# Kernel tuning notes

Measured on AMD Instinct MI355X. Metric: run time of the kernel, lower is better.

## Reference

```python
import jax, jax.numpy as jnp
import numpy as np

B, N, K_H, K_EC = 32, 2048, 50, 5  # graphs, nodes/graph, homophily-knn k, edgeconv k


def _leaky(v):
    return jnp.where(v >= 0, v, 0.01 * v)


def _pairwise_sq(xg):
    # xg: [B,N,F] -> squared euclidean distances [B,N,N]
    s = jnp.sum(xg * xg, axis=-1)
    return s[:, :, None] + s[:, None, :] - 2.0 * jnp.einsum('bnf,bmf->bnm', xg, xg)


def _gather(xg, idx):
    # xg [B,N,F], idx [B,N,k] -> [B,N,k,F]
    return jax.vmap(lambda xs, ix: xs[ix])(xg, idx)


def _edge_conv(xg, w1, b1, w2, b2):
    # DynamicEdgeConv: knn (self included, as PyG knn), msg = nn([x_i, x_j - x_i]), aggr='add'
    d = _pairwise_sq(xg)
    _, idx = jax.lax.top_k(-d, K_EC)          # [B,N,k]
    xj = _gather(xg, idx)                      # [B,N,k,F]
    xi = jnp.broadcast_to(xg[:, :, None, :], xj.shape)
    m = jnp.concatenate([xi, xj - xi], axis=-1)
    h = _leaky(m @ w1 + b1)
    h = _leaky(h @ w2 + b2)
    return h.sum(axis=2)                       # add aggregation -> [B,N,out]


def _homophily(y, idx):
    # y [B,N], idx [B,N,k]: fraction of edges whose endpoints have equal value, per graph
    yj = jax.vmap(lambda ys, ix: ys[ix])(y, idx)
    same = (yj == y[:, :, None]).astype(jnp.float32)
    return same.mean(axis=(1, 2))              # [B]


def reference(x, pos, batch, c1w1, c1b1, c1w2, c1b2, c2w1, c2b1, c2w2, c2b2,
              l1w1, l1b1, l1w2, l1b2, mw1, mb1, mw2, mb2):
    xx = jnp.concatenate([x, pos], axis=1).reshape(B, N, 4)
    # homophily kNN graph (k=50, self-loops excluded as in knn_graph)
    d = _pairwise_sq(xx) + jnp.eye(N, dtype=xx.dtype) * 1e9
    _, hidx = jax.lax.top_k(-d, K_H)
    h = [_homophily(xx[..., c], hidx) for c in range(4)]  # hx,hy,hz,hq each [B]
    x1 = _edge_conv(xx, c1w1, c1b1, c1w2, c1b2)   # [B,N,64]
    x2 = _edge_conv(x1, c2w1, c2b1, c2w2, c2b2)   # shared conv2 weights
    x3 = _edge_conv(x2, c2w1, c2b1, c2w2, c2b2)
    feat = jnp.concatenate([xx, x1, x2, x3], axis=-1)  # [B,N,196]
    o = _leaky(feat @ l1w1 + l1b1) @ l1w2 + l1b2       # lin1 -> [B,N,256]
    o = o.mean(axis=1)                                  # global_mean_pool -> [B,256]
    o = jnp.concatenate([o] + [hh[:, None] for hh in h], axis=1)  # [B,260]
    o = _leaky(o)
    o = _leaky(o @ mw1 + mb1)
    return o @ mw2 + mb2                                # [B,cla]


def setup_inputs() -> dict:
    key = jax.random.key(0)
    ks = jax.random.split(key, 20)

    def lin(k, fin, fout):
        kw, kb = jax.random.split(k)
        s = 1.0 / np.sqrt(fin)
        return (jax.random.uniform(kw, (fin, fout), jnp.float32, -s, s),
                jax.random.uniform(kb, (fout,), jnp.float32, -s, s))

    x = jax.random.normal(ks[0], (B * N, 1), jnp.float32)
    pos = jax.random.normal(ks[1], (B * N, 3), jnp.float32)
    batch = jnp.repeat(jnp.arange(B, dtype=jnp.int64), N)
    c1w1, c1b1 = lin(ks[2], 8, 64)
    c1w2, c1b2 = lin(ks[3], 64, 64)
    c2w1, c2b1 = lin(ks[4], 128, 128)
    c2w2, c2b2 = lin(ks[5], 128, 64)
    l1w1, l1b1 = lin(ks[6], 196, 512)
    l1w2, l1b2 = lin(ks[7], 512, 256)
    mw1, mb1 = lin(ks[8], 260, 256)
    mw2, mb2 = lin(ks[9], 256, 3)
    return dict(x=x, pos=pos, batch=batch,
                c1w1=c1w1, c1b1=c1b1, c1w2=c1w2, c1b2=c1b2,
                c2w1=c2w1, c2b1=c2b1, c2w2=c2w2, c2b2=c2b2,
                l1w1=l1w1, l1b1=l1b1, l1w2=l1w2, l1b2=l1b2,
                mw1=mw1, mb1=mb1, mw2=mw2, mb2=mb2)
```

## Files before the change

### kernel.cpp

```cpp
#include <hip/hip_runtime.h>

static constexpr int B = 32, N = 2048, BN = B * N;

#define DEV static __device__ __forceinline__

typedef _Float16 half_t;
typedef __attribute__((ext_vector_type(8))) _Float16 half8;
typedef __attribute__((ext_vector_type(4))) float f32x4;

DEV float lk(float v) { return v >= 0.f ? v : 0.01f * v; }
DEV bool lexlt(float d1, int j1, float d2, int j2) {
    return d1 < d2 || (d1 == d2 && j1 < j2);
}

DEV unsigned int mono(float f) {
    unsigned int b = __float_as_uint(f);
    return b ^ ((unsigned int)((int)b >> 31) | 0x80000000u);
}
DEV float unmono(unsigned int v) {
    unsigned int b = (v & 0x80000000u) ? (v & 0x7fffffffu) : ~v;
    return __uint_as_float(b);
}
DEV int mbcnt64(unsigned long long m) {
    return __builtin_amdgcn_mbcnt_hi((unsigned)(m >> 32),
                                     __builtin_amdgcn_mbcnt_lo((unsigned)m, 0));
}
DEV float dist4s(float4 a, float sa, float4 b, float sb) {
    float dt = fmaf(a.x, b.x, fmaf(a.y, b.y, fmaf(a.z, b.z, a.w * b.w)));
    return (sa + sb) - 2.f * dt;
}

__global__ __launch_bounds__(256) void k_build_xx(const float* __restrict__ x,
                                                  const float* __restrict__ pos,
                                                  float* __restrict__ xx,
                                                  float* __restrict__ sq) {
    int i = blockIdx.x * 256 + threadIdx.x;
    if (i < BN) {
        float4 v;
        v.x = x[i];
        v.y = pos[3 * i + 0];
        v.z = pos[3 * i + 1];
        v.w = pos[3 * i + 2];
        ((float4*)xx)[i] = v;
        sq[i] = fmaf(v.x, v.x, fmaf(v.y, v.y, fmaf(v.z, v.z, v.w * v.w)));
    }
}

__global__ __launch_bounds__(256, 8) void k_knn4(const float* __restrict__ xx,
                                                 const float* __restrict__ sq,
                                                 int* __restrict__ c1idx,
                                                 unsigned int* __restrict__ hpart) {
    int gw = (blockIdx.x * 256 + threadIdx.x) >> 6;
    int lane = threadIdx.x & 63;
    int g = gw >> 11, i = gw & 2047;
    int lane_self = i & 63, t_self = i >> 6;
    const float4* base = ((const float4*)xx) + g * N;
    const float* sqb = sq + g * N;
    float4 xi = base[i];
    float si = sqb[i];

    unsigned int L[6];
#pragma unroll
    for (int s = 0; s < 6; s++) L[s] = 0xFFFFFFFFu;
#pragma unroll 4
    for (int t = 0; t < 32; t++) {
        float4 xj = base[lane + 64 * t];
        float sj = sqb[lane + 64 * t];
        unsigned int nv = mono(dist4s(xi, si, xj, sj));
#pragma unroll
        for (int s = 0; s < 6; s++) {
            unsigned int lo_ = min(L[s], nv);
            nv = max(L[s], nv);
            L[s] = lo_;
        }
    }
    unsigned int uself = 0x80000000u;

    unsigned int lo = L[0], hi = L[0];
#pragma unroll
    for (int o = 1; o < 64; o <<= 1) {
        lo = min(lo, (unsigned int)__shfl_xor((int)lo, o));
        hi = max(hi, (unsigned int)__shfl_xor((int)hi, o));
    }
    unsigned int cp = lo ^ hi;
    int msb = cp ? (31 - __builtin_clz(cp)) : -1;
    unsigned int prefix = (msb >= 0) ? (hi & ~((2u << msb) - 1u)) : lo;

    unsigned int vA = prefix, vB = prefix;
#pragma unroll 1
    for (int bit = msb; bit >= 0; --bit) {
        unsigned int cA = vA | (1u << bit);
        unsigned int cB = vB | (1u << bit);
        int cntA = 0, cntB = 0;
#pragma unroll
        for (int s = 0; s < 6; s++) cntA += (int)__popcll(__ballot(L[s] < cA));
#pragma unroll
        for (int s = 0; s < 5; s++) cntB += (int)__popcll(__ballot(L[s] < cB));
        cntA -= (uself < cA) ? 1 : 0;
        if (cntA < 50) vA = cA;
        if (cntB < 5) vB = cB;
    }
    if (__ballot(L[5] < vA) != 0ULL) {
        vA = prefix;
#pragma unroll 1
        for (int bit = msb; bit >= 0; --bit) {
            unsigned int c = vA | (1u << bit);
            int cnt = 0;
            for (int t = 0; t < 32; t++) {
                float4 xj = base[lane + 64 * t];
                float sj = sqb[lane + 64 * t];
                unsigned int uv = mono(dist4s(xi, si, xj, sj));
                cnt += (int)__popcll(__ballot(uv < c));
            }
            cnt -= (uself < c) ? 1 : 0;
            if (cnt < 50) vA = c;
        }
    }
    float tA = unmono(vA), tB = unmono(vB);

    unsigned int rawA = 0, eqAm = 0, rawB = 0, eqBm = 0;
#pragma unroll 4
    for (int t = 0; t < 32; t++) {
        float4 xj = base[lane + 64 * t];
        float sj = sqb[lane + 64 * t];
        float dv = dist4s(xi, si, xj, sj);
        rawA |= (dv < tA ? 1u : 0u) << t;
        eqAm |= (dv == tA ? 1u : 0u) << t;
        rawB |= (dv < tB ? 1u : 0u) << t;
        eqBm |= (dv == tB ? 1u : 0u) << t;
    }
    unsigned int packA = (unsigned)__popc(rawA) | ((unsigned)__popc(eqAm) << 16);
    unsigned int packB = (unsigned)__popc(rawB) | ((unsigned)__popc(eqBm) << 16);
#pragma unroll
    for (int o = 1; o < 64; o <<= 1) {
        packA += __shfl_xor(packA, o);
        packB += __shfl_xor(packB, o);
    }
    int cltA = (int)(packA & 0xffffu) - ((uself < vA) ? 1 : 0);
    int ceqA = (int)(packA >> 16) - ((uself == vA) ? 1 : 0);
    int cltB = (int)(packB & 0xffffu);
    int ceqB = (int)(packB >> 16);

    int neededA = 50 - cltA;
    bool allEqA = (ceqA == neededA);
    unsigned int selAm = rawA, eqAs = eqAm;
    if (lane == lane_self) {
        selAm &= ~(1u << t_self);
        eqAs &= ~(1u << t_self);
    }
    unsigned int hm = allEqA ? (selAm | eqAs) : selAm;
    int c0 = 0, c1 = 0, c2 = 0, c3 = 0;
    unsigned int mm = hm;
    while (mm) {
        int t = __ffs(mm) - 1;
        mm &= mm - 1;
        float4 xj = base[lane + 64 * t];
        c0 += (xj.x == xi.x) ? 1 : 0;
        c1 += (xj.y == xi.y) ? 1 : 0;
        c2 += (xj.z == xi.z) ? 1 : 0;
        c3 += (xj.w == xi.w) ? 1 : 0;
    }
    if (!allEqA) {
        unsigned int em = eqAs;
        for (int r = 0; r < neededA; r++) {
            int mt = __ffs(em) - 1;
            int mj = (mt >= 0) ? (lane + 64 * mt) : 0x7fffffff;
            int bm = mj;
#pragma unroll
            for (int o = 1; o < 64; o <<= 1) bm = min(bm, __shfl_xor(bm, o));
            if (mj == bm && mt >= 0) {
                em &= ~(1u << mt);
                float4 xj = base[lane + 64 * mt];
                c0 += (xj.x == xi.x) ? 1 : 0;
                c1 += (xj.y == xi.y) ? 1 : 0;
                c2 += (xj.z == xi.z) ? 1 : 0;
                c3 += (xj.w == xi.w) ? 1 : 0;
            }
        }
    }
    unsigned int pc = (unsigned)c0 | ((unsigned)c1 << 8) | ((unsigned)c2 << 16) | ((unsigned)c3 << 24);
#pragma unroll
    for (int o = 1; o < 64; o <<= 1) pc += __shfl_xor(pc, o);
    if (lane == 0) hpart[gw] = pc;

    int neededB = 5 - cltB;
    bool allEqB = (ceqB == neededB);
    unsigned int selBm = allEqB ? (rawB | eqBm) : rawB;
    int base_slot = 0;
#pragma unroll 4
    for (int t = 0; t < 32; t++) {
        bool take = (selBm >> t) & 1;
        unsigned long long m = __ballot(take);
        if (take) c1idx[gw * 5 + base_slot + mbcnt64(m)] = lane + 64 * t;
        base_slot += (int)__popcll(m);
    }
    if (!allEqB) {
        unsigned int em = eqBm;
        for (int r = 0; r < neededB; r++) {
            int mt = __ffs(em) - 1;
            int mj = (mt >= 0) ? (lane + 64 * mt) : 0x7fffffff;
            int bm = mj;
#pragma unroll
            for (int o = 1; o < 64; o <<= 1) bm = min(bm, __shfl_xor(bm, o));
            if (mj == bm && mt >= 0) {
                em &= ~(1u << mt);
                c1idx[gw * 5 + base_slot + r] = bm;
            }
        }
    }
}

__global__ __launch_bounds__(256) void k_split(const float* __restrict__ X,
                                               half_t* __restrict__ Xh,
                                               half_t* __restrict__ Xl,
                                               float* __restrict__ s) {
    int row = (blockIdx.x * 256 + threadIdx.x) >> 6;
    int lane = threadIdx.x & 63;
    float x = X[(size_t)row * 64 + lane];
    half_t h = (half_t)x;
    half_t l = (half_t)(x - (float)h);
    Xh[(size_t)row * 64 + lane] = h;
    Xl[(size_t)row * 64 + lane] = l;
    float ss = x * x;
#pragma unroll
    for (int o = 1; o < 64; o <<= 1) ss += __shfl_xor(ss, o);
    if (lane == 0) s[row] = ss;
}

template <int F, int C>
__global__ __launch_bounds__(256, 4) void k_pq(const float* __restrict__ X,
                                               const float* __restrict__ w1,
                                               const float* __restrict__ b1,
                                               float* __restrict__ p,
                                               float* __restrict__ q) {
    constexpr int FS = F + 4;
    __shared__ __align__(16) float Xs[64 * FS];
    __shared__ __align__(16) float Ws[64 * FS];
    int nbase = blockIdx.x * 64;
    int cchunk = blockIdx.y;
    int tx = threadIdx.x & 15, ty = threadIdx.x >> 4;
    for (int idx = threadIdx.x; idx < 64 * (F / 4); idx += 256) {
        int r = idx / (F / 4), fq = idx % (F / 4);
        float4 v = ((const float4*)(X + (size_t)(nbase + r) * F))[fq];
        *(float4*)&Xs[r * FS + fq * 4] = v;
    }
    for (int idx = threadIdx.x; idx < 64 * F; idx += 256) {
        int f = idx >> 6, cl = idx & 63;
        int ccg = cchunk * 64 + cl;
        float v;
        if (ccg < C) v = w1[f * C + ccg] - w1[(F + f) * C + ccg];
        else         v = w1[(F + f) * C + (ccg - C)];
        Ws[cl * FS + f] = v;
    }
    __syncthreads();
    float acc[4][4];
#pragma unroll
    for (int a = 0; a < 4; a++)
#pragma unroll
        for (int b = 0; b < 4; b++) acc[a][b] = 0.f;
#pragma unroll 2
    for (int fs = 0; fs < F / 4; fs++) {
        float4 xv[4], wv[4];
#pragma unroll
        for (int a = 0; a < 4; a++) xv[a] = *(const float4*)&Xs[(ty + 16 * a) * FS + fs * 4];
#pragma unroll
        for (int b = 0; b < 4; b++) wv[b] = *(const float4*)&Ws[(tx + 16 * b) * FS + fs * 4];
#pragma unroll
        for (int a = 0; a < 4; a++)
#pragma unroll
            for (int b = 0; b < 4; b++) {
                acc[a][b] = fmaf(xv[a].x, wv[b].x, acc[a][b]);
                acc[a][b] = fmaf(xv[a].y, wv[b].y, acc[a][b]);
                acc[a][b] = fmaf(xv[a].z, wv[b].z, acc[a][b]);
                acc[a][b] = fmaf(xv[a].w, wv[b].w, acc[a][b]);
            }
    }
#pragma unroll
    for (int a = 0; a < 4; a++) {
        int n = nbase + ty + 16 * a;
#pragma unroll
        for (int b = 0; b < 4; b++) {
            int ccg = cchunk * 64 + tx + 16 * b;
            if (ccg < C) p[(size_t)n * C + ccg] = acc[a][b] + b1[ccg];
            else         q[(size_t)n * C + (ccg - C)] = acc[a][b];
        }
    }
}

template <int C1>
__global__ __launch_bounds__(256, 4) void k_edge(const float* __restrict__ p,
                                                 const float* __restrict__ q,
                                                 const int* __restrict__ cidx,
                                                 const float* __restrict__ w2,
                                                 const float* __restrict__ b2,
                                                 float* __restrict__ Xout) {
    __shared__ __align__(16) float h1[80 * 68];
    __shared__ __align__(16) float w2T[64 * 68];
    int nb = blockIdx.x * 16;
    int gb = (nb >> 11) << 11;
    int tx = threadIdx.x & 15, ty = threadIdx.x >> 4;
    float acc[5][4];
#pragma unroll
    for (int m = 0; m < 5; m++)
#pragma unroll
        for (int n = 0; n < 4; n++) acc[m][n] = 0.f;
#pragma unroll 1
    for (int half = 0; half < C1 / 64; half++) {
        __syncthreads();
        for (int idx = threadIdx.x; idx < 64 * 64; idx += 256) {
            int l = idx >> 6, c = idx & 63;
            w2T[c * 68 + l] = w2[(half * 64 + l) * 64 + c];
        }
        for (int idx = threadIdx.x; idx < 80 * 16; idx += 256) {
            int e = idx >> 4, fq = idx & 15;
            int node = nb + e / 5, kk = e - 5 * (e / 5);
            int j = cidx[node * 5 + kk];
            float4 pv = ((const float4*)(p + (size_t)node * C1 + half * 64))[fq];
            float4 qv = ((const float4*)(q + (size_t)(gb + j) * C1 + half * 64))[fq];
            float4 hv;
            hv.x = lk(pv.x + qv.x); hv.y = lk(pv.y + qv.y);
            hv.z = lk(pv.z + qv.z); hv.w = lk(pv.w + qv.w);
            *(float4*)&h1[e * 68 + fq * 4] = hv;
        }
        __syncthreads();
#pragma unroll 1
        for (int ls = 0; ls < 16; ls++) {
            float4 hv[5], wf[4];
#pragma unroll
            for (int m = 0; m < 5; m++) hv[m] = *(const float4*)&h1[(ty + 16 * m) * 68 + ls * 4];
#pragma unroll
            for (int n = 0; n < 4; n++) wf[n] = *(const float4*)&w2T[(tx + 16 * n) * 68 + ls * 4];
#pragma unroll
            for (int m = 0; m < 5; m++)
#pragma unroll
                for (int n = 0; n < 4; n++) {
                    acc[m][n] = fmaf(hv[m].x, wf[n].x, acc[m][n]);
                    acc[m][n] = fmaf(hv[m].y, wf[n].y, acc[m][n]);
                    acc[m][n] = fmaf(hv[m].z, wf[n].z, acc[m][n]);
                    acc[m][n] = fmaf(hv[m].w, wf[n].w, acc[m][n]);
                }
        }
    }
    float b2r[4];
#pragma unroll
    for (int n = 0; n < 4; n++) b2r[n] = b2[tx + 16 * n];
    __syncthreads();
    float* h2 = h1;
#pragma unroll
    for (int m = 0; m < 5; m++)
#pragma unroll
        for (int n = 0; n < 4; n++)
            h2[(ty + 16 * m) * 68 + (tx + 16 * n)] = lk(acc[m][n] + b2r[n]);
    __syncthreads();
#pragma unroll
    for (int rr = 0; rr < 4; rr++) {
        int idx = threadIdx.x + 256 * rr;
        int node = idx >> 6, c = idx & 63;
        float sum = 0.f;
#pragma unroll
        for (int kk = 0; kk < 5; kk++) sum += h2[(node * 5 + kk) * 68 + c];
        Xout[(size_t)(nb + node) * 64 + c] = sum;
    }
}

__global__ __launch_bounds__(256) void k_knn64(const half_t* __restrict__ Xh,
                                               const half_t* __restrict__ Xl,
                                               const float* __restrict__ s,
                                               float2* __restrict__ cand) {
    __shared__ __align__(16) char smem[30720];
    half_t* XjH = (half_t*)smem;
    half_t* XjL = (half_t*)(smem + 9216);
    float* sJ = (float*)(smem + 18432);
    int g = blockIdx.x, it = blockIdx.y, bz = blockIdx.z;
    int gbase = g * 2048, ibase = it * 64;
    int lane = threadIdx.x & 63, wave = threadIdx.x >> 6;
    int m = lane & 15, quad = lane >> 4;

    {
        const half_t* ah = Xh + (size_t)(gbase + ibase + wave * 16 + m) * 64 + quad * 8;
        const half_t* al = Xl + (size_t)(gbase + ibase + wave * 16 + m) * 64 + quad * 8;
    }
    const half_t* ahp = Xh + (size_t)(gbase + ibase + wave * 16 + m) * 64 + quad * 8;
    const half_t* alp = Xl + (size_t)(gbase + ibase + wave * 16 + m) * 64 + quad * 8;
    half8 Ah0 = *(const half8*)(ahp);
    half8 Ah1 = *(const half8*)(ahp + 32);
    half8 Al0 = *(const half8*)(alp);
    half8 Al1 = *(const half8*)(alp + 32);
    float si_r[4];
#pragma unroll
    for (int reg = 0; reg < 4; reg++)
        si_r[reg] = s[gbase + ibase + wave * 16 + quad * 4 + reg];

    float t5v[4][5];
    int t5j[4][5];
    float thv[4];
#pragma unroll
    for (int a = 0; a < 4; a++) {
        thv[a] = __builtin_inff();
#pragma unroll
        for (int ss = 0; ss < 5; ss++) { t5v[a][ss] = __builtin_inff(); t5j[a][ss] = 0x7fffffff; }
    }

    int jt0 = bz * 16;
#pragma unroll 1
    for (int jtl = 0; jtl < 16; jtl++) {
        int jt = jt0 + jtl;
        __syncthreads();
        for (int idx = threadIdx.x; idx < 512; idx += 256) {
            int r = idx >> 3, c = idx & 7;
            *(half8*)&XjH[r * 72 + c * 8] = *(const half8*)(Xh + (size_t)(gbase + jt * 64 + r) * 64 + c * 8);
            *(half8*)&XjL[r * 72 + c * 8] = *(const half8*)(Xl + (size_t)(gbase + jt * 64 + r) * 64 + c * 8);
        }
        if (threadIdx.x < 64) sJ[threadIdx.x] = s[gbase + jt * 64 + threadIdx.x];
        __syncthreads();
        if ((jtl & 3) == 0) {
#pragma unroll
            for (int reg = 0; reg < 4; reg++) {
                float th = t5v[reg][4];
                th = fminf(th, __shfl_xor(th, 1));
                th = fminf(th, __shfl_xor(th, 2));
                th = fminf(th, __shfl_xor(th, 4));
                th = fminf(th, __shfl_xor(th, 8));
                thv[reg] = th;
            }
        }
#pragma unroll
        for (int sub = 0; sub < 4; sub++) {
            int brow = (sub * 16 + m) * 72 + quad * 8;
            half8 Bh0 = *(const half8*)&XjH[brow];
            half8 Bh1 = *(const half8*)&XjH[brow + 32];
            half8 Bl0 = *(const half8*)&XjL[brow];
            half8 Bl1 = *(const half8*)&XjL[brow + 32];
            f32x4 ahh = {0.f, 0.f, 0.f, 0.f};
            f32x4 ahl = {0.f, 0.f, 0.f, 0.f};
            f32x4 alh = {0.f, 0.f, 0.f, 0.f};
            f32x4 all = {0.f, 0.f, 0.f, 0.f};
            ahh = __builtin_amdgcn_mfma_f32_16x16x32_f16(Ah0, Bh0, ahh, 0, 0, 0);
            ahl = __builtin_amdgcn_mfma_f32_16x16x32_f16(Ah0, Bl0, ahl, 0, 0, 0);
            alh = __builtin_amdgcn_mfma_f32_16x16x32_f16(Al0, Bh0, alh, 0, 0, 0);
            all = __builtin_amdgcn_mfma_f32_16x16x32_f16(Al0, Bl0, all, 0, 0, 0);
            ahh = __builtin_amdgcn_mfma_f32_16x16x32_f16(Ah1, Bh1, ahh, 0, 0, 0);
            ahl = __builtin_amdgcn_mfma_f32_16x16x32_f16(Ah1, Bl1, ahl, 0, 0, 0);
            alh = __builtin_amdgcn_mfma_f32_16x16x32_f16(Al1, Bh1, alh, 0, 0, 0);
            all = __builtin_amdgcn_mfma_f32_16x16x32_f16(Al1, Bl1, all, 0, 0, 0);
            float sjv = sJ[sub * 16 + m];
            int jv = jt * 64 + sub * 16 + m;
#pragma unroll
            for (int reg = 0; reg < 4; reg++) {
                float dot = ((all[reg] + alh[reg]) + ahl[reg]) + ahh[reg];
                float dv = (si_r[reg] + sjv) - 2.f * dot;
                if (dv <= thv[reg]) {
                    if (lexlt(dv, jv, t5v[reg][4], t5j[reg][4])) {
                        t5v[reg][4] = dv; t5j[reg][4] = jv;
#pragma unroll
                        for (int ss = 4; ss >= 1; ss--)
                            if (lexlt(t5v[reg][ss], t5j[reg][ss], t5v[reg][ss - 1], t5j[reg][ss - 1])) {
                                float tv = t5v[reg][ss]; t5v[reg][ss] = t5v[reg][ss - 1]; t5v[reg][ss - 1] = tv;
                                int tj = t5j[reg][ss]; t5j[reg][ss] = t5j[reg][ss - 1]; t5j[reg][ss - 1] = tj;
                            }
                    }
                }
            }
        }
    }

    float* candd = (float*)smem;
    unsigned short* candj = (unsigned short*)(smem + 20480);
    __syncthreads();
    int rowbase = wave * 16 + quad * 4;
#pragma unroll
    for (int reg = 0; reg < 4; reg++)
#pragma unroll
        for (int ss = 0; ss < 5; ss++) {
            candd[(rowbase + reg) * 80 + m * 5 + ss] = t5v[reg][ss];
            candj[(rowbase + reg) * 80 + m * 5 + ss] = (unsigned short)t5j[reg][ss];
        }
    __syncthreads();
    if (threadIdx.x < 64) {
        int row = threadIdx.x;
        float fv[5];
        int fj[5];
#pragma unroll
        for (int ss = 0; ss < 5; ss++) { fv[ss] = __builtin_inff(); fj[ss] = 0x7fffffff; }
#pragma unroll 1
        for (int c = 0; c < 80; c++) {
            float dv = candd[row * 80 + c];
            int jv = (int)candj[row * 80 + c];
            if (lexlt(dv, jv, fv[4], fj[4])) {
                fv[4] = dv; fj[4] = jv;
#pragma unroll
                for (int ss = 4; ss >= 1; ss--)
                    if (lexlt(fv[ss], fj[ss], fv[ss - 1], fj[ss - 1])) {
                        float tv = fv[ss]; fv[ss] = fv[ss - 1]; fv[ss - 1] = tv;
                        int tj = fj[ss]; fj[ss] = fj[ss - 1]; fj[ss - 1] = tj;
                    }
            }
        }
#pragma unroll
        for (int ss = 0; ss < 5; ss++) {
            float2 e;
            e.x = fv[ss];
            e.y = __int_as_float(fj[ss]);
            cand[((size_t)(gbase + ibase + row) * 2 + bz) * 5 + ss] = e;
        }
    }
}

__global__ __launch_bounds__(256) void k_knn_merge(const float2* __restrict__ cand,
                                                   int* __restrict__ cidx) {
    int row = blockIdx.x * 256 + threadIdx.x;
    if (row >= BN) return;
    float fv[5];
    int fj[5];
#pragma unroll
    for (int ss = 0; ss < 5; ss++) { fv[ss] = __builtin_inff(); fj[ss] = 0x7fffffff; }
#pragma unroll
    for (int c = 0; c < 10; c++) {
        float2 e = cand[(size_t)row * 10 + c];
        float dv = e.x;
        int jv = __float_as_int(e.y);
        if (lexlt(dv, jv, fv[4], fj[4])) {
            fv[4] = dv; fj[4] = jv;
#pragma unroll
            for (int ss = 4; ss >= 1; ss--)
                if (lexlt(fv[ss], fj[ss], fv[ss - 1], fj[ss - 1])) {
                    float tv = fv[ss]; fv[ss] = fv[ss - 1]; fv[ss - 1] = tv;
                    int tj = fj[ss]; fj[ss] = fj[ss - 1]; fj[ss - 1] = tj;
                }
        }
    }
#pragma unroll
    for (int ss = 0; ss < 5; ss++) cidx[(size_t)row * 5 + ss] = fj[ss];
}

__global__ __launch_bounds__(256, 3) void k_lin1(const float* __restrict__ xx,
                                                 const float* __restrict__ x1,
                                                 const float* __restrict__ x2,
                                                 const float* __restrict__ x3,
                                                 const float* __restrict__ w1,
                                                 const float* __restrict__ b1,
                                                 float* __restrict__ Hpart) {
    __shared__ __align__(16) float ft[64 * 100];
    __shared__ __align__(16) float wT[64 * 100];
    int cch = blockIdx.x, g = blockIdx.y, z = blockIdx.z;
    int gbase = g * 2048;
    int tx = threadIdx.x & 15, ty = threadIdx.x >> 4;
    float accp[4][4][4];
#pragma unroll
    for (int nt = 0; nt < 4; nt++)
#pragma unroll
        for (int rm = 0; rm < 4; rm++)
#pragma unroll
            for (int ca = 0; ca < 4; ca++) accp[nt][rm][ca] = 0.f;
#pragma unroll 1
    for (int half = 0; half < 2; half++) {
        int FH = half ? 96 : 100;
        __syncthreads();
        for (int idx = threadIdx.x; idx < 64 * 100; idx += 256) {
            int f = idx >> 6, cl = idx & 63;
            if (f < FH) wT[cl * 100 + f] = w1[(half * 100 + f) * 512 + cch * 64 + cl];
        }
        int NF4 = half ? 24 : 25;
#pragma unroll 1
        for (int nt = 0; nt < 4; nt++) {
            int n0 = (z * 4 + nt) * 64;
            __syncthreads();
            for (int idx = threadIdx.x; idx < 64 * NF4; idx += 256) {
                int r = idx / NF4, fq = idx - r * NF4;
                int node = gbase + n0 + r;
                float4 v;
                if (half == 0) {
                    if (fq == 0)      v = ((const float4*)(xx + (size_t)node * 4))[0];
                    else if (fq < 17) v = ((const float4*)(x1 + (size_t)node * 64))[fq - 1];
                    else              v = ((const float4*)(x2 + (size_t)node * 64))[fq - 17];
                } else {
                    if (fq < 8)       v = ((const float4*)(x2 + (size_t)node * 64))[fq + 8];
                    else              v = ((const float4*)(x3 + (size_t)node * 64))[fq - 8];
                }
                *(float4*)&ft[r * 100 + fq * 4] = v;
            }
            __syncthreads();
            int FSN = NF4;
#pragma unroll 2
            for (int fs = 0; fs < FSN; fs++) {
                float4 fv[4], wv[4];
#pragma unroll
                for (int rm = 0; rm < 4; rm++) fv[rm] = *(const float4*)&ft[(ty + 16 * rm) * 100 + fs * 4];
#pragma unroll
                for (int ca = 0; ca < 4; ca++) wv[ca] = *(const float4*)&wT[(tx + 16 * ca) * 100 + fs * 4];
#pragma unroll
                for (int rm = 0; rm < 4; rm++)
#pragma unroll
                    for (int ca = 0; ca < 4; ca++) {
                        accp[nt][rm][ca] = fmaf(fv[rm].x, wv[ca].x, accp[nt][rm][ca]);
                        accp[nt][rm][ca] = fmaf(fv[rm].y, wv[ca].y, accp[nt][rm][ca]);
                        accp[nt][rm][ca] = fmaf(fv[rm].z, wv[ca].z, accp[nt][rm][ca]);
                        accp[nt][rm][ca] = fmaf(fv[rm].w, wv[ca].w, accp[nt][rm][ca]);
                    }
            }
        }
    }
    float b1r[4];
#pragma unroll
    for (int ca = 0; ca < 4; ca++) b1r[ca] = b1[cch * 64 + tx + 16 * ca];
    float psum[4] = {0.f, 0.f, 0.f, 0.f};
#pragma unroll
    for (int nt = 0; nt < 4; nt++)
#pragma unroll
        for (int rm = 0; rm < 4; rm++)
#pragma unroll
            for (int ca = 0; ca < 4; ca++) psum[ca] += lk(accp[nt][rm][ca] + b1r[ca]);
    __syncthreads();
    float* red = ft;
#pragma unroll
    for (int ca = 0; ca < 4; ca++) red[ty * 64 + tx + 16 * ca] = psum[ca];
    __syncthreads();
    if (threadIdx.x < 64) {
        float tot = 0.f;
#pragma unroll
        for (int t = 0; t < 16; t++) tot += red[t * 64 + threadIdx.x];
        Hpart[((size_t)z * 32 + g) * 512 + cch * 64 + threadIdx.x] = tot;
    }
}

__global__ __launch_bounds__(256) void k_final(const float* __restrict__ Hpart,
                                               const unsigned int* __restrict__ hpart,
                                               const float* __restrict__ l1w2,
                                               const float* __restrict__ l1b2,
                                               const float* __restrict__ mw1,
                                               const float* __restrict__ mb1,
                                               const float* __restrict__ mw2,
                                               const float* __restrict__ mb2,
                                               float* __restrict__ out) {
    __shared__ float Hb[512];
    __shared__ float z[260];
    __shared__ float y[256];
    __shared__ unsigned int hsum[4];
    int g = blockIdx.x, t = threadIdx.x;
    if (t < 4) hsum[t] = 0;
    __syncthreads();
    unsigned int s0 = 0, s1 = 0, s2 = 0, s3 = 0;
#pragma unroll
    for (int r = 0; r < 8; r++) {
        unsigned int v = hpart[g * 2048 + t + 256 * r];
        s0 += v & 0xffu; s1 += (v >> 8) & 0xffu;
        s2 += (v >> 16) & 0xffu; s3 += (v >> 24) & 0xffu;
    }
    atomicAdd(&hsum[0], s0); atomicAdd(&hsum[1], s1);
    atomicAdd(&hsum[2], s2); atomicAdd(&hsum[3], s3);
#pragma unroll
    for (int half = 0; half < 2; half++) {
        int c = t + 256 * half;
        float v = 0.f;
#pragma unroll
        for (int zz = 0; zz < 8; zz++) v += Hpart[((size_t)zz * 32 + g) * 512 + c];
        Hb[c] = v * (1.f / 2048.f);
    }
    __syncthreads();
    float acc = l1b2[t];
    for (int f = 0; f < 512; f++) acc = fmaf(Hb[f], l1w2[f * 256 + t], acc);
    z[t] = lk(acc);
    if (t < 4) z[256 + t] = lk((float)hsum[t] * (1.f / (2048.f * 50.f)));
    __syncthreads();
    float acc2 = mb1[t];
    for (int f = 0; f < 260; f++) acc2 = fmaf(z[f], mw1[f * 256 + t], acc2);
    y[t] = lk(acc2);
    __syncthreads();
    if (t < 3) {
        float a = mb2[t];
        for (int c = 0; c < 256; c++) a = fmaf(y[c], mw2[c * 3 + t], a);
        out[g * 3 + t] = a;
    }
}

extern "C" void kernel_launch(void* const* d_in, const int* in_sizes, int n_in,
                              void* d_out, int out_size, void* d_ws, size_t ws_size,
                              hipStream_t stream) {
    (void)in_sizes; (void)n_in; (void)out_size; (void)ws_size;
    const float* x    = (const float*)d_in[0];
    const float* pos  = (const float*)d_in[1];
    const float* c1w1 = (const float*)d_in[3];
    const float* c1b1 = (const float*)d_in[4];
    const float* c1w2 = (const float*)d_in[5];
    const float* c1b2 = (const float*)d_in[6];
    const float* c2w1 = (const float*)d_in[7];
    const float* c2b1 = (const float*)d_in[8];
    const float* c2w2 = (const float*)d_in[9];
    const float* c2b2 = (const float*)d_in[10];
    const float* l1w1 = (const float*)d_in[11];
    const float* l1b1 = (const float*)d_in[12];
    const float* l1w2 = (const float*)d_in[13];
    const float* l1b2 = (const float*)d_in[14];
    const float* mw1  = (const float*)d_in[15];
    const float* mb1  = (const float*)d_in[16];
    const float* mw2  = (const float*)d_in[17];
    const float* mb2  = (const float*)d_in[18];
    float* out = (float*)d_out;

    char* w = (char*)d_ws;
    auto alloc = [&](size_t bytes) -> void* {
        void* r = (void*)w;
        w += (bytes + 255) & ~(size_t)255;
        return r;
    };
    float* xx   = (float*)alloc((size_t)BN * 4 * 4);
    float* pbuf = (float*)alloc((size_t)BN * 128 * 4);
    float* qbuf = (float*)alloc((size_t)BN * 128 * 4);
    float* x1   = (float*)alloc((size_t)BN * 64 * 4);
    float* x2   = (float*)alloc((size_t)BN * 64 * 4);
    float* x3   = (float*)alloc((size_t)BN * 64 * 4);
    float* sbuf = (float*)alloc((size_t)BN * 4);
    float* sq4  = (float*)alloc((size_t)BN * 4);
    half_t* xh  = (half_t*)alloc((size_t)BN * 64 * 2);
    half_t* xl  = (half_t*)alloc((size_t)BN * 64 * 2);
    int* c1i    = (int*)alloc((size_t)BN * 5 * 4);
    int* c2i    = (int*)alloc((size_t)BN * 5 * 4);
    int* c3i    = (int*)alloc((size_t)BN * 5 * 4);
    unsigned int* hpart = (unsigned int*)alloc((size_t)BN * 4);
    float* Hpart = (float*)alloc((size_t)8 * 32 * 512 * 4);
    float2* cand = (float2*)alloc((size_t)BN * 10 * 8);

    k_build_xx<<<BN / 256, 256, 0, stream>>>(x, pos, xx, sq4);
    k_knn4<<<BN / 4, 256, 0, stream>>>(xx, sq4, c1i, hpart);
    k_pq<4, 64><<<dim3(BN / 64, 2), 256, 0, stream>>>(xx, c1w1, c1b1, pbuf, qbuf);
    k_edge<64><<<BN / 16, 256, 0, stream>>>(pbuf, qbuf, c1i, c1w2, c1b2, x1);
    k_split<<<BN / 4, 256, 0, stream>>>(x1, xh, xl, sbuf);
    k_knn64<<<dim3(32, 32, 2), 256, 0, stream>>>(xh, xl, sbuf, cand);
    k_knn_merge<<<BN / 256, 256, 0, stream>>>(cand, c2i);
    k_pq<64, 128><<<dim3(BN / 64, 4), 256, 0, stream>>>(x1, c2w1, c2b1, pbuf, qbuf);
    k_edge<128><<<BN / 16, 256, 0, stream>>>(pbuf, qbuf, c2i, c2w2, c2b2, x2);
    k_split<<<BN / 4, 256, 0, stream>>>(x2, xh, xl, sbuf);
    k_knn64<<<dim3(32, 32, 2), 256, 0, stream>>>(xh, xl, sbuf, cand);
    k_knn_merge<<<BN / 256, 256, 0, stream>>>(cand, c3i);
    k_pq<64, 128><<<dim3(BN / 64, 4), 256, 0, stream>>>(x2, c2w1, c2b1, pbuf, qbuf);
    k_edge<128><<<BN / 16, 256, 0, stream>>>(pbuf, qbuf, c3i, c2w2, c2b2, x3);
    k_lin1<<<dim3(8, 32, 8), 256, 0, stream>>>(xx, x1, x2, x3, l1w1, l1b1, Hpart);
    k_final<<<32, 256, 0, stream>>>(Hpart, hpart, l1w2, l1b2, mw1, mb1, mw2, mb2, out);
}
```

Measured before the change: 1.678 ms.

## Skip homophily kNN when no coordinate matches, cache distances, split knn64 four ways

The homophily kNN kernel now keeps all 32 per-lane distance keys in registers and records whether any non-self point shares a coordinate value with the query. When no such point exists, the homophily count is exactly zero, so the k=50 threshold search, selection and counting are skipped and only the k=5 edge-conv search runs. The 64-dim kNN kernel splits the candidate range into four z-slices instead of two, merges adjacent-lane top-5 lists with shuffles before the shared-memory merge, and uses less shared memory. The merge kernel now reads twenty candidates per row. The trade-offs are higher register pressure from the cached distance array and more candidate traffic through global memory.

```diff
diff --git a/kernel.cpp b/kernel.cpp
--- a/kernel.cpp
+++ b/kernel.cpp
@@ -16,10 +16,6 @@
 DEV unsigned int mono(float f) {
     unsigned int b = __float_as_uint(f);
     return b ^ ((unsigned int)((int)b >> 31) | 0x80000000u);
-}
-DEV float unmono(unsigned int v) {
-    unsigned int b = (v & 0x80000000u) ? (v & 0x7fffffffu) : ~v;
-    return __uint_as_float(b);
 }
 DEV int mbcnt64(unsigned long long m) {
     return __builtin_amdgcn_mbcnt_hi((unsigned)(m >> 32),
@@ -59,7 +55,9 @@
     float4 xi = base[i];
     float si = sqb[i];
 
+    unsigned int u[32];
     unsigned int L[6];
+    unsigned int eqany = 0;
 #pragma unroll
     for (int s = 0; s < 6; s++) L[s] = 0xFFFFFFFFu;
 #pragma unroll 4
@@ -67,6 +65,10 @@
         float4 xj = base[lane + 64 * t];
         float sj = sqb[lane + 64 * t];
         unsigned int nv = mono(dist4s(xi, si, xj, sj));
+        u[t] = nv;
+        bool eq = (xj.x == xi.x) | (xj.y == xi.y) | (xj.z == xi.z) | (xj.w == xi.w);
+        bool notself = (lane + 64 * t) != i;
+        eqany |= (eq && notself) ? (1u << t) : 0u;
 #pragma unroll
         for (int s = 0; s < 6; s++) {
             unsigned int lo_ = min(L[s], nv);
@@ -75,6 +77,7 @@
         }
     }
     unsigned int uself = 0x80000000u;
+    bool haveEq = (__ballot(eqany != 0) != 0ULL);
 
     unsigned int lo = L[0], hi = L[0];
 #pragma unroll
@@ -87,102 +90,113 @@
     unsigned int prefix = (msb >= 0) ? (hi & ~((2u << msb) - 1u)) : lo;
 
     unsigned int vA = prefix, vB = prefix;
-#pragma unroll 1
-    for (int bit = msb; bit >= 0; --bit) {
-        unsigned int cA = vA | (1u << bit);
-        unsigned int cB = vB | (1u << bit);
-        int cntA = 0, cntB = 0;
-#pragma unroll
-        for (int s = 0; s < 6; s++) cntA += (int)__popcll(__ballot(L[s] < cA));
-#pragma unroll
-        for (int s = 0; s < 5; s++) cntB += (int)__popcll(__ballot(L[s] < cB));
-        cntA -= (uself < cA) ? 1 : 0;
-        if (cntA < 50) vA = cA;
-        if (cntB < 5) vB = cB;
-    }
-    if (__ballot(L[5] < vA) != 0ULL) {
-        vA = prefix;
+    if (haveEq) {
 #pragma unroll 1
         for (int bit = msb; bit >= 0; --bit) {
-            unsigned int c = vA | (1u << bit);
-            int cnt = 0;
-            for (int t = 0; t < 32; t++) {
-                float4 xj = base[lane + 64 * t];
-                float sj = sqb[lane + 64 * t];
-                unsigned int uv = mono(dist4s(xi, si, xj, sj));
-                cnt += (int)__popcll(__ballot(uv < c));
-            }
-            cnt -= (uself < c) ? 1 : 0;
-            if (cnt < 50) vA = c;
-        }
-    }
-    float tA = unmono(vA), tB = unmono(vB);
-
-    unsigned int rawA = 0, eqAm = 0, rawB = 0, eqBm = 0;
-#pragma unroll 4
+            unsigned int cA = vA | (1u << bit);
+            unsigned int cB = vB | (1u << bit);
+            int cntA = 0, cntB = 0;
+#pragma unroll
+            for (int s = 0; s < 6; s++) cntA += (int)__popcll(__ballot(L[s] < cA));
+#pragma unroll
+            for (int s = 0; s < 5; s++) cntB += (int)__popcll(__ballot(L[s] < cB));
+            cntA -= (uself < cA) ? 1 : 0;
+            if (cntA < 50) vA = cA;
+            if (cntB < 5) vB = cB;
+        }
+        if (__ballot(L[5] < vA) != 0ULL) {
+            vA = prefix;
+#pragma unroll 1
+            for (int bit = msb; bit >= 0; --bit) {
+                unsigned int c = vA | (1u << bit);
+                int cnt = 0;
+#pragma unroll
+                for (int t = 0; t < 32; t++) cnt += (int)__popcll(__ballot(u[t] < c));
+                cnt -= (uself < c) ? 1 : 0;
+                if (cnt < 50) vA = c;
+            }
+        }
+    } else {
+#pragma unroll 1
+        for (int bit = msb; bit >= 0; --bit) {
+            unsigned int cB = vB | (1u << bit);
+            int cntB = 0;
+#pragma unroll
+            for (int s = 0; s < 5; s++) cntB += (int)__popcll(__ballot(L[s] < cB));
+            if (cntB < 5) vB = cB;
+        }
+    }
+
+    unsigned int rawB = 0, eqBm = 0;
+#pragma unroll
     for (int t = 0; t < 32; t++) {
-        float4 xj = base[lane + 64 * t];
-        float sj = sqb[lane + 64 * t];
-        float dv = dist4s(xi, si, xj, sj);
-        rawA |= (dv < tA ? 1u : 0u) << t;
-        eqAm |= (dv == tA ? 1u : 0u) << t;
-        rawB |= (dv < tB ? 1u : 0u) << t;
-        eqBm |= (dv == tB ? 1u : 0u) << t;
-    }
-    unsigned int packA = (unsigned)__popc(rawA) | ((unsigned)__popc(eqAm) << 16);
+        rawB |= (u[t] < vB ? 1u : 0u) << t;
+        eqBm |= (u[t] == vB ? 1u : 0u) << t;
+    }
     unsigned int packB = (unsigned)__popc(rawB) | ((unsigned)__popc(eqBm) << 16);
-#pragma unroll
-    for (int o = 1; o < 64; o <<= 1) {
-        packA += __shfl_xor(packA, o);
-        packB += __shfl_xor(packB, o);
-    }
-    int cltA = (int)(packA & 0xffffu) - ((uself < vA) ? 1 : 0);
-    int ceqA = (int)(packA >> 16) - ((uself == vA) ? 1 : 0);
+
+    if (haveEq) {
+        unsigned int rawA = 0, eqAm = 0;
+#pragma unroll
+        for (int t = 0; t < 32; t++) {
+            rawA |= (u[t] < vA ? 1u : 0u) << t;
+            eqAm |= (u[t] == vA ? 1u : 0u) << t;
+        }
+        unsigned int packA = (unsigned)__popc(rawA) | ((unsigned)__popc(eqAm) << 16);
+#pragma unroll
+        for (int o = 1; o < 64; o <<= 1) packA += __shfl_xor(packA, o);
+        int cltA = (int)(packA & 0xffffu) - ((uself < vA) ? 1 : 0);
+        int ceqA = (int)(packA >> 16) - ((uself == vA) ? 1 : 0);
+
+        int neededA = 50 - cltA;
+        bool allEqA = (ceqA == neededA);
+        unsigned int selAm = rawA, eqAs = eqAm;
+        if (lane == lane_self) {
+            selAm &= ~(1u << t_self);
+            eqAs &= ~(1u << t_self);
+        }
+        unsigned int hm = allEqA ? (selAm | eqAs) : selAm;
+        int c0 = 0, c1 = 0, c2 = 0, c3 = 0;
+        unsigned int mm = hm;
+        while (mm) {
+            int t = __ffs(mm) - 1;
+            mm &= mm - 1;
+            float4 xj = base[lane + 64 * t];
+            c0 += (xj.x == xi.x) ? 1 : 0;
+            c1 += (xj.y == xi.y) ? 1 : 0;
+            c2 += (xj.z == xi.z) ? 1 : 0;
+            c3 += (xj.w == xi.w) ? 1 : 0;
+        }
+        if (!allEqA) {
+            unsigned int em = eqAs;
+            for (int r = 0; r < neededA; r++) {
+                int mt = __ffs(em) - 1;
+                int mj = (mt >= 0) ? (lane + 64 * mt) : 0x7fffffff;
+                int bm = mj;
+#pragma unroll
+                for (int o = 1; o < 64; o <<= 1) bm = min(bm, __shfl_xor(bm, o));
+                if (mj == bm && mt >= 0) {
+                    em &= ~(1u << mt);
+                    float4 xj = base[lane + 64 * mt];
+                    c0 += (xj.x == xi.x) ? 1 : 0;
+                    c1 += (xj.y == xi.y) ? 1 : 0;
+                    c2 += (xj.z == xi.z) ? 1 : 0;
+                    c3 += (xj.w == xi.w) ? 1 : 0;
+                }
+            }
+        }
+        unsigned int pc = (unsigned)c0 | ((unsigned)c1 << 8) | ((unsigned)c2 << 16) | ((unsigned)c3 << 24);
+#pragma unroll
+        for (int o = 1; o < 64; o <<= 1) pc += __shfl_xor(pc, o);
+        if (lane == 0) hpart[gw] = pc;
+    } else {
+        if (lane == 0) hpart[gw] = 0u;
+    }
+
+#pragma unroll
+    for (int o = 1; o < 64; o <<= 1) packB += __shfl_xor(packB, o);
     int cltB = (int)(packB & 0xffffu);
     int ceqB = (int)(packB >> 16);
-
-    int neededA = 50 - cltA;
-    bool allEqA = (ceqA == neededA);
-    unsigned int selAm = rawA, eqAs = eqAm;
-    if (lane == lane_self) {
-        selAm &= ~(1u << t_self);
-        eqAs &= ~(1u << t_self);
-    }
-    unsigned int hm = allEqA ? (selAm | eqAs) : selAm;
-    int c0 = 0, c1 = 0, c2 = 0, c3 = 0;
-    unsigned int mm = hm;
-    while (mm) {
-        int t = __ffs(mm) - 1;
-        mm &= mm - 1;
-        float4 xj = base[lane + 64 * t];
-        c0 += (xj.x == xi.x) ? 1 : 0;
-        c1 += (xj.y == xi.y) ? 1 : 0;
-        c2 += (xj.z == xi.z) ? 1 : 0;
-        c3 += (xj.w == xi.w) ? 1 : 0;
-    }
-    if (!allEqA) {
-        unsigned int em = eqAs;
-        for (int r = 0; r < neededA; r++) {
-            int mt = __ffs(em) - 1;
-            int mj = (mt >= 0) ? (lane + 64 * mt) : 0x7fffffff;
-            int bm = mj;
-#pragma unroll
-            for (int o = 1; o < 64; o <<= 1) bm = min(bm, __shfl_xor(bm, o));
-            if (mj == bm && mt >= 0) {
-                em &= ~(1u << mt);
-                float4 xj = base[lane + 64 * mt];
-                c0 += (xj.x == xi.x) ? 1 : 0;
-                c1 += (xj.y == xi.y) ? 1 : 0;
-                c2 += (xj.z == xi.z) ? 1 : 0;
-                c3 += (xj.w == xi.w) ? 1 : 0;
-            }
-        }
-    }
-    unsigned int pc = (unsigned)c0 | ((unsigned)c1 << 8) | ((unsigned)c2 << 16) | ((unsigned)c3 << 24);
-#pragma unroll
-    for (int o = 1; o < 64; o <<= 1) pc += __shfl_xor(pc, o);
-    if (lane == 0) hpart[gw] = pc;
-
     int neededB = 5 - cltB;
     bool allEqB = (ceqB == neededB);
     unsigned int selBm = allEqB ? (rawB | eqBm) : rawB;
@@ -367,7 +381,7 @@
                                                const half_t* __restrict__ Xl,
                                                const float* __restrict__ s,
                                                float2* __restrict__ cand) {
-    __shared__ __align__(16) char smem[30720];
+    __shared__ __align__(16) char smem[18688];
     half_t* XjH = (half_t*)smem;
     half_t* XjL = (half_t*)(smem + 9216);
     float* sJ = (float*)(smem + 18432);
@@ -376,10 +390,6 @@
     int lane = threadIdx.x & 63, wave = threadIdx.x >> 6;
     int m = lane & 15, quad = lane >> 4;
 
-    {
-        const half_t* ah = Xh + (size_t)(gbase + ibase + wave * 16 + m) * 64 + quad * 8;
-        const half_t* al = Xl + (size_t)(gbase + ibase + wave * 16 + m) * 64 + quad * 8;
-    }
     const half_t* ahp = Xh + (size_t)(gbase + ibase + wave * 16 + m) * 64 + quad * 8;
     const half_t* alp = Xl + (size_t)(gbase + ibase + wave * 16 + m) * 64 + quad * 8;
     half8 Ah0 = *(const half8*)(ahp);
@@ -401,9 +411,9 @@
         for (int ss = 0; ss < 5; ss++) { t5v[a][ss] = __builtin_inff(); t5j[a][ss] = 0x7fffffff; }
     }
 
-    int jt0 = bz * 16;
-#pragma unroll 1
-    for (int jtl = 0; jtl < 16; jtl++) {
+    int jt0 = bz * 8;
+#pragma unroll 1
+    for (int jtl = 0; jtl < 8; jtl++) {
         int jt = jt0 + jtl;
         __syncthreads();
         for (int idx = threadIdx.x; idx < 512; idx += 256) {
@@ -464,17 +474,43 @@
         }
     }
 
+#pragma unroll
+    for (int reg = 0; reg < 4; reg++) {
+        float pv[5]; int pj[5];
+#pragma unroll
+        for (int ss = 0; ss < 5; ss++) {
+            pv[ss] = __shfl_xor(t5v[reg][ss], 1);
+            pj[ss] = __shfl_xor(t5j[reg][ss], 1);
+        }
+        if ((lane & 1) == 0) {
+#pragma unroll
+            for (int c = 0; c < 5; c++) {
+                if (lexlt(pv[c], pj[c], t5v[reg][4], t5j[reg][4])) {
+                    t5v[reg][4] = pv[c]; t5j[reg][4] = pj[c];
+#pragma unroll
+                    for (int ss = 4; ss >= 1; ss--)
+                        if (lexlt(t5v[reg][ss], t5j[reg][ss], t5v[reg][ss - 1], t5j[reg][ss - 1])) {
+                            float tv = t5v[reg][ss]; t5v[reg][ss] = t5v[reg][ss - 1]; t5v[reg][ss - 1] = tv;
+                            int tj = t5j[reg][ss]; t5j[reg][ss] = t5j[reg][ss - 1]; t5j[reg][ss - 1] = tj;
+                        }
+                }
+            }
+        }
+    }
+
     float* candd = (float*)smem;
-    unsigned short* candj = (unsigned short*)(smem + 20480);
+    unsigned short* candj = (unsigned short*)(smem + 10240);
     __syncthreads();
     int rowbase = wave * 16 + quad * 4;
-#pragma unroll
-    for (int reg = 0; reg < 4; reg++)
-#pragma unroll
-        for (int ss = 0; ss < 5; ss++) {
-            candd[(rowbase + reg) * 80 + m * 5 + ss] = t5v[reg][ss];
-            candj[(rowbase + reg) * 80 + m * 5 + ss] = (unsigned short)t5j[reg][ss];
-        }
+    if ((lane & 1) == 0) {
+#pragma unroll
+        for (int reg = 0; reg < 4; reg++)
+#pragma unroll
+            for (int ss = 0; ss < 5; ss++) {
+                candd[(rowbase + reg) * 40 + (m >> 1) * 5 + ss] = t5v[reg][ss];
+                candj[(rowbase + reg) * 40 + (m >> 1) * 5 + ss] = (unsigned short)t5j[reg][ss];
+            }
+    }
     __syncthreads();
     if (threadIdx.x < 64) {
         int row = threadIdx.x;
@@ -483,9 +519,9 @@
 #pragma unroll
         for (int ss = 0; ss < 5; ss++) { fv[ss] = __builtin_inff(); fj[ss] = 0x7fffffff; }
 #pragma unroll 1
-        for (int c = 0; c < 80; c++) {
-            float dv = candd[row * 80 + c];
-            int jv = (int)candj[row * 80 + c];
+        for (int c = 0; c < 40; c++) {
+            float dv = candd[row * 40 + c];
+            int jv = (int)candj[row * 40 + c];
             if (lexlt(dv, jv, fv[4], fj[4])) {
                 fv[4] = dv; fj[4] = jv;
 #pragma unroll
@@ -501,7 +537,7 @@
             float2 e;
             e.x = fv[ss];
             e.y = __int_as_float(fj[ss]);
-            cand[((size_t)(gbase + ibase + row) * 2 + bz) * 5 + ss] = e;
+            cand[((size_t)(gbase + ibase + row) * 4 + bz) * 5 + ss] = e;
         }
     }
 }
@@ -515,8 +551,8 @@
 #pragma unroll
     for (int ss = 0; ss < 5; ss++) { fv[ss] = __builtin_inff(); fj[ss] = 0x7fffffff; }
 #pragma unroll
-    for (int c = 0; c < 10; c++) {
-        float2 e = cand[(size_t)row * 10 + c];
+    for (int c = 0; c < 20; c++) {
+        float2 e = cand[(size_t)row * 20 + c];
         float dv = e.x;
         int jv = __float_as_int(e.y);
         if (lexlt(dv, jv, fv[4], fj[4])) {
@@ -718,19 +754,19 @@
     int* c3i    = (int*)alloc((size_t)BN * 5 * 4);
     unsigned int* hpart = (unsigned int*)alloc((size_t)BN * 4);
     float* Hpart = (float*)alloc((size_t)8 * 32 * 512 * 4);
-    float2* cand = (float2*)alloc((size_t)BN * 10 * 8);
+    float2* cand = (float2*)alloc((size_t)BN * 20 * 8);
 
     k_build_xx<<<BN / 256, 256, 0, stream>>>(x, pos, xx, sq4);
     k_knn4<<<BN / 4, 256, 0, stream>>>(xx, sq4, c1i, hpart);
     k_pq<4, 64><<<dim3(BN / 64, 2), 256, 0, stream>>>(xx, c1w1, c1b1, pbuf, qbuf);
     k_edge<64><<<BN / 16, 256, 0, stream>>>(pbuf, qbuf, c1i, c1w2, c1b2, x1);
     k_split<<<BN / 4, 256, 0, stream>>>(x1, xh, xl, sbuf);
-    k_knn64<<<dim3(32, 32, 2), 256, 0, stream>>>(xh, xl, sbuf, cand);
+    k_knn64<<<dim3(32, 32, 4), 256, 0, stream>>>(xh, xl, sbuf, cand);
     k_knn_merge<<<BN / 256, 256, 0, stream>>>(cand, c2i);
     k_pq<64, 128><<<dim3(BN / 64, 4), 256, 0, stream>>>(x1, c2w1, c2b1, pbuf, qbuf);
     k_edge<128><<<BN / 16, 256, 0, stream>>>(pbuf, qbuf, c2i, c2w2, c2b2, x2);
     k_split<<<BN / 4, 256, 0, stream>>>(x2, xh, xl, sbuf);
-    k_knn64<<<dim3(32, 32, 2), 256, 0, stream>>>(xh, xl, sbuf, cand);
+    k_knn64<<<dim3(32, 32, 4), 256, 0, stream>>>(xh, xl, sbuf, cand);
     k_knn_merge<<<BN / 256, 256, 0, stream>>>(cand, c3i);
     k_pq<64, 128><<<dim3(BN / 64, 4), 256, 0, stream>>>(x2, c2w1, c2b1, pbuf, qbuf);
     k_edge<128><<<BN / 16, 256, 0, stream>>>(pbuf, qbuf, c3i, c2w2, c2b2, x3);
```

Measured after the change: 1.658 ms. About the same (-1.2%).
